# Kernel tuning notes

Hardware: AMD Instinct MI355X
Metric: run time of the kernel (lower is better)

Reference implementation:

```python
import jax, jax.numpy as jnp
import numpy as np

# Static problem sizes
N, NS, E, B = 6000, 20000, 60000, 16   # atoms, subgraph nodes, subgraph edges, molecules
IN_DIM, EMB, HID = 78, 1024, 2048
H = 4                 # GAT heads
C = HID // H          # 512 per-head channels
L = 3                 # num GAT layers
LN_EPS = 1e-5
SM_EPS = 1e-16        # PyG softmax denominator eps


def setup_inputs() -> dict:
    key = jax.random.key(0)
    ks = jax.random.split(key, 20)
    g = lambda k, shape, s: jax.random.normal(k, shape, jnp.float32) * s
    inp = {}
    inp["x"] = jax.random.uniform(ks[0], (N, IN_DIM), jnp.float32)
    inp["subgraph_edge_attr"] = jnp.ones((E, 1), jnp.float32)
    inp["Wn"] = g(ks[1], (IN_DIM, EMB), 0.1)
    inp["bn"] = g(ks[2], (EMB,), 0.02)
    inp["We"] = g(ks[3], (1, EMB), 0.1)
    inp["be"] = g(ks[4], (EMB,), 0.02)
    inp["W0"] = g(ks[5], (EMB, HID), EMB ** -0.5)
    inp["Ws"] = g(ks[6], (L - 1, HID, HID), HID ** -0.5)
    inp["att_src"] = g(ks[7], (L, H, C), C ** -0.5)
    inp["att_dst"] = g(ks[8], (L, H, C), C ** -0.5)
    inp["att_edge"] = g(ks[9], (L, H, C), C ** -0.5)
    inp["W_edge"] = g(ks[10], (L, EMB, HID), EMB ** -0.5)
    inp["conv_bias"] = g(ks[11], (L, HID), 0.02)
    inp["gamma"] = jnp.ones((L, HID), jnp.float32)
    inp["beta"] = jnp.zeros((L, HID), jnp.float32)
    inp["Wf"] = g(ks[12], (HID, HID), HID ** -0.5)
    inp["bf"] = g(ks[13], (HID,), 0.02)
    inp["subgraph_node_index"] = jax.random.randint(ks[14], (NS,), 0, N)
    inp["subgraph_edge_index"] = jax.random.randint(ks[15], (2, E), 0, NS)
    inp["subgraph_indicator"] = jax.random.randint(ks[16], (NS,), 0, N)
    inp["batch_index"] = jnp.sort(jax.random.randint(ks[17], (N,), 0, B))
    return inp


def _layernorm(h, g, b):
    mu = h.mean(-1, keepdims=True)
    v = jnp.square(h - mu).mean(-1, keepdims=True)
    return (h - mu) * jax.lax.rsqrt(v + LN_EPS) * g + b


def _gat_conv(h, Win, e_emb, a_src, a_dst, a_edge, We_l, bias, src, dst, n_nodes):
    # h: [n, in]; e_emb: [Et, EMB]; a_*: [H, C]
    xh = (h @ Win).reshape(-1, H, C)                       # [n, H, C]
    s_src = (xh * a_src).sum(-1)                           # [n, H]
    s_dst = (xh * a_dst).sum(-1)                           # [n, H]
    eh = (e_emb @ We_l).reshape(-1, H, C)                  # [Et, H, C]
    s_edge = (eh * a_edge).sum(-1)                         # [Et, H]
    logits = jax.nn.leaky_relu(s_src[src] + s_dst[dst] + s_edge, 0.2)
    # softmax over incoming edges of each destination node, per head
    m = jax.ops.segment_max(logits, dst, num_segments=n_nodes)
    p = jnp.exp(logits - m[dst])
    z = jax.ops.segment_sum(p, dst, num_segments=n_nodes)
    alpha = p / (z[dst] + SM_EPS)                          # [Et, H]
    msg = xh[src] * alpha[:, :, None]                      # [Et, H, C]
    out = jax.ops.segment_sum(msg, dst, num_segments=n_nodes)
    return out.reshape(-1, H * C) + bias                   # [n, HID]


def reference(x, subgraph_edge_attr, Wn, bn, We, be, W0, Ws, att_src, att_dst,
              att_edge, W_edge, conv_bias, gamma, beta, Wf, bf,
              subgraph_node_index, subgraph_edge_index, subgraph_indicator,
              batch_index):
    n_sub = subgraph_node_index.shape[0]
    n_nodes = x.shape[0]
    # node_projection + gather into subgraph-node space
    h = (x @ Wn + bn)[subgraph_node_index]                 # [NS, EMB]
    # edge_encoder
    e = subgraph_edge_attr @ We + be                       # [E, EMB]
    src = subgraph_edge_index[0]
    dst = subgraph_edge_index[1]
    # PyG GATConv add_self_loops with fill_value='mean' on encoded edge attrs
    loop = jnp.arange(n_sub)
    src = jnp.concatenate([src, loop])
    dst = jnp.concatenate([dst, loop])
    e_loop = jnp.broadcast_to(e.mean(axis=0, keepdims=True), (n_sub, e.shape[1]))
    e = jnp.concatenate([e, e_loop], axis=0)               # [E+NS, EMB]
    for i in range(L):
        Win = W0 if i == 0 else Ws[i - 1]
        h = _gat_conv(h, Win, e, att_src[i], att_dst[i], att_edge[i],
                      W_edge[i], conv_bias[i], src, dst, n_sub)
        h = jax.nn.relu(_layernorm(h, gamma[i], beta[i]))
    # subgraph mean aggregation back to atoms (index_add + bincount clamp(1))
    agg = jax.ops.segment_sum(h, subgraph_indicator, num_segments=n_nodes)
    cnt = jax.ops.segment_sum(jnp.ones((n_sub,), h.dtype), subgraph_indicator,
                              num_segments=n_nodes)
    agg = agg / jnp.maximum(cnt, 1.0)[:, None]
    out_nodes = agg @ Wf + bf                              # final_projection
    # global_mean_pool over molecules
    pooled = jax.ops.segment_sum(out_nodes, batch_index, num_segments=B)
    gcnt = jax.ops.segment_sum(jnp.ones((n_nodes,), h.dtype), batch_index,
                               num_segments=B)
    return pooled / jnp.maximum(gcnt, 1.0)[:, None]        # [B, HID]
```

## Files before the change

kernel.cpp:

```cpp
#include <hip/hip_runtime.h>

typedef unsigned short ushortT;
typedef __attribute__((ext_vector_type(4))) float f32x4;
typedef __attribute__((ext_vector_type(8))) short bf16x8;
typedef __attribute__((ext_vector_type(4))) unsigned int u32x4;
typedef __attribute__((ext_vector_type(4))) unsigned short u16x4;

#define N_ATOMS 6000
#define NSUB    20000
#define NEDGE   60000
#define NBATCH  16
#define INDIM   78
#define EMB     1024
#define HID     2048
#define NH      4
#define CH      512
#define NL      3
#define MP      20096
#define AP      6016
#define ETOT    (NEDGE + NSUB)
#define NPB     8

#define GLOAD_LDS16(gp, lp) \
    __builtin_amdgcn_global_load_lds((const __attribute__((address_space(1))) void*)(gp), \
                                     (__attribute__((address_space(3))) void*)(lp), 16, 0, 0)

__device__ __forceinline__ ushortT f2bf(float x) {
    union { float f; unsigned u; } v; v.f = x;
    unsigned r = v.u + 0x7fffu + ((v.u >> 16) & 1u);
    return (ushortT)(r >> 16);
}
__device__ __forceinline__ float bf2f(ushortT h) {
    union { unsigned u; float f; } v; v.u = ((unsigned)h) << 16; return v.f;
}

__global__ void k_cast_transpose(const float* __restrict__ W, ushortT* __restrict__ Wt,
                                 int K, int Nn) {
    __shared__ float tile[32][33];
    int n0 = blockIdx.x * 32, k0 = blockIdx.y * 32;
    int tx = threadIdx.x, ty = threadIdx.y;
    for (int i = 0; i < 32; i += 8)
        tile[ty + i][tx] = W[(size_t)(k0 + ty + i) * Nn + n0 + tx];
    __syncthreads();
    for (int i = 0; i < 32; i += 8)
        Wt[(size_t)(n0 + ty + i) * K + k0 + tx] = f2bf(tile[tx][ty + i]);
}

__global__ __launch_bounds__(256) void k_node_proj(const float* __restrict__ x,
                                                   const float* __restrict__ Wn,
                                                   const float* __restrict__ bn,
                                                   ushortT* __restrict__ xpb) {
    int n0 = blockIdx.x * NPB;
    __shared__ float xr[NPB][INDIM];
    int tid = threadIdx.x;
    for (int i = tid; i < NPB * INDIM; i += 256)
        xr[i / INDIM][i % INDIM] = x[(size_t)(n0 + i / INDIM) * INDIM + (i % INDIM)];
    __syncthreads();
    for (int j = tid; j < EMB; j += 256) {
        float acc[NPB];
        float b = bn[j];
        #pragma unroll
        for (int a = 0; a < NPB; ++a) acc[a] = b;
        #pragma unroll 6
        for (int k = 0; k < INDIM; ++k) {
            float wv = Wn[(size_t)k * EMB + j];
            #pragma unroll
            for (int a = 0; a < NPB; ++a) acc[a] += xr[a][k] * wv;
        }
        #pragma unroll
        for (int a = 0; a < NPB; ++a)
            xpb[(size_t)(n0 + a) * EMB + j] = f2bf(acc[a]);
    }
}

__global__ void k_mean_part(const float* __restrict__ ea, float* __restrict__ mpart) {
    __shared__ float red[256];
    int b = blockIdx.x;
    float s = 0;
    for (int i = b * 256 + threadIdx.x; i < NEDGE; i += 64 * 256) s += ea[i];
    red[threadIdx.x] = s; __syncthreads();
    for (int d = 128; d > 0; d >>= 1) {
        if (threadIdx.x < d) red[threadIdx.x] += red[threadIdx.x + d];
        __syncthreads();
    }
    if (threadIdx.x == 0) mpart[b] = red[0];
}

__global__ void k_eprep(const int* __restrict__ srci, const int* __restrict__ sni,
                        const float* __restrict__ ea, const float* __restrict__ meana,
                        int* __restrict__ esrcS, int* __restrict__ esrcA,
                        float* __restrict__ eaf) {
    int t = blockIdx.x * 256 + threadIdx.x;
    if (t >= ETOT) return;
    int s = (t < NEDGE) ? srci[t] : (t - NEDGE);
    esrcS[t] = s;
    esrcA[t] = sni[s];
    eaf[t] = (t < NEDGE) ? ea[t] : meana[0];
}

__global__ __launch_bounds__(256) void k_pq_part(const float* __restrict__ We,
                                                 const float* __restrict__ be,
                                                 const float* __restrict__ W_edge,
                                                 const float* __restrict__ att_edge,
                                                 float* __restrict__ part) {
    int l = blockIdx.x >> 2, h = blockIdx.x & 3;
    int k0 = blockIdx.y * 64;
    const float* Wl = W_edge + (size_t)l * EMB * HID + h * CH;
    const float* ae = att_edge + ((size_t)l * NH + h) * CH;
    int tid = threadIdx.x;
    float aP0 = 0, aP1 = 0, aQ0 = 0, aQ1 = 0;
    #pragma unroll 4
    for (int k = k0; k < k0 + 64; ++k) {
        float wek = We[k], bek = be[k];
        float w0 = Wl[(size_t)k * HID + tid];
        float w1 = Wl[(size_t)k * HID + tid + 256];
        aP0 += wek * w0; aP1 += wek * w1;
        aQ0 += bek * w0; aQ1 += bek * w1;
    }
    float p = aP0 * ae[tid] + aP1 * ae[tid + 256];
    float q = aQ0 * ae[tid] + aQ1 * ae[tid + 256];
    __shared__ float rp[256], rq[256];
    rp[tid] = p; rq[tid] = q; __syncthreads();
    for (int d = 128; d > 0; d >>= 1) {
        if (tid < d) { rp[tid] += rp[tid + d]; rq[tid] += rq[tid + d]; }
        __syncthreads();
    }
    if (tid == 0) {
        part[((size_t)blockIdx.y * 12 + blockIdx.x) * 2]     = rp[0];
        part[((size_t)blockIdx.y * 12 + blockIdx.x) * 2 + 1] = rq[0];
    }
}

__global__ void k_pq_red(const float* __restrict__ part, const float* __restrict__ mpart,
                         float* __restrict__ pq, float* __restrict__ meana) {
    int t = threadIdx.x;
    if (t < 24) {
        float s = 0;
        for (int kc = 0; kc < 16; ++kc) s += part[((size_t)kc * 12 + (t >> 1)) * 2 + (t & 1)];
        pq[t] = s;
    }
    if (t == 32) {
        float s = 0;
        for (int i = 0; i < 64; ++i) s += mpart[i];
        meana[0] = s / (float)NEDGE;
    }
}

__global__ void k_count(const int* __restrict__ dsti, int* __restrict__ cnt) {
    int t = blockIdx.x * 256 + threadIdx.x;
    if (t >= ETOT) return;
    int d = (t < NEDGE) ? dsti[t] : (t - NEDGE);
    atomicAdd(&cnt[d], 1);
}

__global__ void k_scan(const int* __restrict__ cnt, int* __restrict__ rs, int n) {
    __shared__ int part[1024];
    int tid = threadIdx.x;
    const int per = (n + 1023) / 1024;
    int base = tid * per;
    int s = 0;
    for (int i = 0; i < per; ++i) { int idx = base + i; if (idx < n) s += cnt[idx]; }
    part[tid] = s;
    __syncthreads();
    for (int d = 1; d < 1024; d <<= 1) {
        int v = (tid >= d) ? part[tid - d] : 0;
        __syncthreads();
        part[tid] += v;
        __syncthreads();
    }
    int off = part[tid] - s;
    for (int i = 0; i < per; ++i) {
        int idx = base + i;
        if (idx < n) { rs[idx] = off; off += cnt[idx]; }
    }
    if (tid == 1023) rs[n] = part[1023];
}

__global__ void k_fill(const int* __restrict__ dsti, const int* __restrict__ rs,
                       int* __restrict__ cursor, int* __restrict__ eids) {
    int t = blockIdx.x * 256 + threadIdx.x;
    if (t >= ETOT) return;
    int d = (t < NEDGE) ? dsti[t] : (t - NEDGE);
    int pos = rs[d] + atomicAdd(&cursor[d], 1);
    eids[pos] = t;
}

__global__ void k_count_ind(const int* __restrict__ ind, int* __restrict__ cnt) {
    int i = blockIdx.x * 256 + threadIdx.x;
    if (i < NSUB) atomicAdd(&cnt[ind[i]], 1);
}

__global__ void k_fill_ind(const int* __restrict__ ind, const int* __restrict__ rs,
                           int* __restrict__ cursor, int* __restrict__ ids) {
    int i = blockIdx.x * 256 + threadIdx.x;
    if (i >= NSUB) return;
    int a = ind[i];
    int pos = rs[a] + atomicAdd(&cursor[a], 1);
    ids[pos] = i;
}

__global__ __launch_bounds__(256) void k_gemm(const ushortT* __restrict__ A,
                                              const ushortT* __restrict__ Bt,
                                              ushortT* __restrict__ Cb, int K) {
    __shared__ alignas(16) ushortT As[128 * 64];
    __shared__ alignas(16) ushortT Bs[128 * 64];
    const int tid = threadIdx.x;
    const int nx = (int)gridDim.x;
    const int ny = (int)gridDim.y;
    int o = (int)blockIdx.y * nx + (int)blockIdx.x;
    int cpx = (nx * ny) >> 3;
    int s = (o & 7) * cpx + (o >> 3);
    const int bm = s / ny, bn = s % ny;
    const int wave = tid >> 6, lane = tid & 63;
    const int wr = wave >> 1, wc = wave & 1;
    f32x4 acc[4][4] = {};
    const int frow = lane & 15;
    const int cb0  = lane >> 4;
    const ushortT* Ab = A + (size_t)bm * 128 * K;
    const ushortT* Bb = Bt + (size_t)bn * 128 * K;
    const int srow = (lane >> 3);
    const int sswz = (((lane & 7) ^ srow) << 3);
    for (int k0 = 0; k0 < K; k0 += 64) {
        #pragma unroll
        for (int i = 0; i < 4; ++i) {
            int c = wave * 4 + i;
            int r = c * 8 + srow;
            GLOAD_LDS16(Ab + (size_t)r * K + k0 + sswz, As + c * 512 + lane * 8);
            GLOAD_LDS16(Bb + (size_t)r * K + k0 + sswz, Bs + c * 512 + lane * 8);
        }
        __syncthreads();
        #pragma unroll
        for (int kk = 0; kk < 64; kk += 32) {
            bf16x8 af[4], bfr[4];
            #pragma unroll
            for (int m = 0; m < 4; ++m) {
                int row = wr * 64 + m * 16 + frow;
                int cb = (kk >> 3) + cb0;
                af[m] = *(const bf16x8*)&As[row * 64 + ((cb ^ (frow & 7)) << 3)];
            }
            #pragma unroll
            for (int n = 0; n < 4; ++n) {
                int row = wc * 64 + n * 16 + frow;
                int cb = (kk >> 3) + cb0;
                bfr[n] = *(const bf16x8*)&Bs[row * 64 + ((cb ^ (frow & 7)) << 3)];
            }
            #pragma unroll
            for (int m = 0; m < 4; ++m)
                #pragma unroll
                for (int n = 0; n < 4; ++n)
                    acc[m][n] = __builtin_amdgcn_mfma_f32_16x16x32_bf16(af[m], bfr[n], acc[m][n], 0, 0, 0);
        }
        __syncthreads();
    }
    const int cr = (lane >> 4) * 4;
    const int cc = lane & 15;
    #pragma unroll
    for (int m = 0; m < 4; ++m)
        #pragma unroll
        for (int n = 0; n < 4; ++n)
            #pragma unroll
            for (int r = 0; r < 4; ++r) {
                size_t row = (size_t)bm * 128 + wr * 64 + m * 16 + cr + r;
                int col = bn * 128 + wc * 64 + n * 16 + cc;
                Cb[row * HID + col] = f2bf(acc[m][n][r]);
            }
}

__global__ __launch_bounds__(256) void k_sdots(const ushortT* __restrict__ xh,
                                               const float* __restrict__ att_src,
                                               const float* __restrict__ att_dst,
                                               float* __restrict__ ssrc,
                                               float* __restrict__ sdst, int layer) {
    int n = blockIdx.x;
    int h = threadIdx.x >> 6, lane = threadIdx.x & 63;
    const ushortT* row = xh + (size_t)n * HID + h * CH + lane * 8;
    const float* as = att_src + ((size_t)layer * NH + h) * CH + lane * 8;
    const float* ad = att_dst + ((size_t)layer * NH + h) * CH + lane * 8;
    u16x4 v0 = *(const u16x4*)row, v1 = *(const u16x4*)(row + 4);
    f32x4 a0 = *(const f32x4*)as, a1 = *(const f32x4*)(as + 4);
    f32x4 d0 = *(const f32x4*)ad, d1 = *(const f32x4*)(ad + 4);
    float ps = 0.f, pd = 0.f;
    #pragma unroll
    for (int t = 0; t < 4; ++t) {
        float f0 = bf2f(v0[t]), f1 = bf2f(v1[t]);
        ps += f0 * a0[t] + f1 * a1[t];
        pd += f0 * d0[t] + f1 * d1[t];
    }
    #pragma unroll
    for (int d = 32; d > 0; d >>= 1) { ps += __shfl_down(ps, d); pd += __shfl_down(pd, d); }
    if (lane == 0) { ssrc[n * NH + h] = ps; sdst[n * NH + h] = pd; }
}

__global__ __launch_bounds__(256) void k_attn(const ushortT* __restrict__ xh,
                                              const float* __restrict__ ssrc,
                                              const float* __restrict__ sdst,
                                              const int* __restrict__ rs,
                                              const int* __restrict__ eids,
                                              const int* __restrict__ esrc,
                                              const float* __restrict__ eaf,
                                              const float* __restrict__ pq,
                                              const float* __restrict__ conv_bias,
                                              const float* __restrict__ gammav,
                                              const float* __restrict__ betav,
                                              ushortT* __restrict__ hout, int layer,
                                              const int* __restrict__ nmap) {
    int wv = threadIdx.x >> 6, lane = threadIdx.x & 63;
    int n = blockIdx.x * 4 + wv;
    int nn = nmap ? nmap[n] : n;
    int beg = rs[n], end = rs[n + 1];
    float px[NH], qx[NH], sd[NH], m[NH], z[NH];
    #pragma unroll
    for (int h = 0; h < NH; ++h) {
        px[h] = pq[(layer * NH + h) * 2];
        qx[h] = pq[(layer * NH + h) * 2 + 1];
        sd[h] = sdst[nn * NH + h];
        m[h] = -INFINITY; z[h] = 0.f;
    }
    float facc[NH][8] = {};
    for (int pos = beg; pos < end; ++pos) {
        int t = eids[pos];
        int s = esrc[t];
        float a = eaf[t];
        const ushortT* xr = xh + (size_t)s * HID + lane * 8;
        #pragma unroll
        for (int h = 0; h < NH; ++h) {
            float logit = ssrc[s * NH + h] + sd[h] + a * px[h] + qx[h];
            logit = (logit > 0.f) ? logit : 0.2f * logit;
            float mn = fmaxf(m[h], logit);
            float scale = expf(m[h] - mn);
            float w = expf(logit - mn);
            z[h] = z[h] * scale + w;
            bf16x8 u = *(const bf16x8*)(xr + h * CH);
            #pragma unroll
            for (int j = 0; j < 8; ++j)
                facc[h][j] = facc[h][j] * scale + w * bf2f((ushortT)u[j]);
            m[h] = mn;
        }
    }
    float val[NH][8];
    float s1 = 0.f, s2 = 0.f;
    #pragma unroll
    for (int h = 0; h < NH; ++h) {
        float inv = 1.f / (z[h] + 1e-16f);
        int cb = h * CH + lane * 8;
        f32x4 b0 = *(const f32x4*)&conv_bias[layer * HID + cb];
        f32x4 b1 = *(const f32x4*)&conv_bias[layer * HID + cb + 4];
        #pragma unroll
        for (int j = 0; j < 4; ++j) {
            float v0 = facc[h][j] * inv + b0[j];
            float v1 = facc[h][4 + j] * inv + b1[j];
            val[h][j] = v0; val[h][4 + j] = v1;
            s1 += v0 + v1; s2 += v0 * v0 + v1 * v1;
        }
    }
    #pragma unroll
    for (int d = 32; d > 0; d >>= 1) { s1 += __shfl_xor(s1, d); s2 += __shfl_xor(s2, d); }
    float mu = s1 / (float)HID;
    float var = s2 / (float)HID - mu * mu;
    float rstd = rsqrtf(var + 1e-5f);
    #pragma unroll
    for (int h = 0; h < NH; ++h) {
        int cb = h * CH + lane * 8;
        f32x4 g0 = *(const f32x4*)&gammav[layer * HID + cb];
        f32x4 g1 = *(const f32x4*)&gammav[layer * HID + cb + 4];
        f32x4 e0 = *(const f32x4*)&betav[layer * HID + cb];
        f32x4 e1 = *(const f32x4*)&betav[layer * HID + cb + 4];
        u16x4 o0, o1;
        #pragma unroll
        for (int j = 0; j < 4; ++j) {
            float y0 = (val[h][j] - mu) * rstd * g0[j] + e0[j];
            float y1 = (val[h][4 + j] - mu) * rstd * g1[j] + e1[j];
            o0[j] = f2bf(fmaxf(y0, 0.f));
            o1[j] = f2bf(fmaxf(y1, 0.f));
        }
        *(u16x4*)&hout[(size_t)n * HID + cb]     = o0;
        *(u16x4*)&hout[(size_t)n * HID + cb + 4] = o1;
    }
}

__global__ __launch_bounds__(256) void k_agg(const ushortT* __restrict__ hbf,
                                             const int* __restrict__ rs2,
                                             const int* __restrict__ ids2,
                                             float* __restrict__ agg) {
    int a = blockIdx.x;
    int beg = rs2[a], end = rs2[a + 1];
    int col = threadIdx.x * 8;
    float acc[8] = {0,0,0,0,0,0,0,0};
    for (int pos = beg; pos < end; ++pos) {
        int i = ids2[pos];
        const u16x4* ptr = (const u16x4*)(hbf + (size_t)i * HID + col);
        u16x4 h0 = ptr[0], h1 = ptr[1];
        #pragma unroll
        for (int t = 0; t < 4; ++t) { acc[t] += bf2f(h0[t]); acc[4 + t] += bf2f(h1[t]); }
    }
    int cnt = end - beg;
    float inv = 1.f / (float)(cnt > 1 ? cnt : 1);
    f32x4 o0, o1;
    #pragma unroll
    for (int t = 0; t < 4; ++t) { o0[t] = acc[t] * inv; o1[t] = acc[4 + t] * inv; }
    float* dst = agg + (size_t)a * HID + col;
    *(f32x4*)dst = o0;
    *(f32x4*)(dst + 4) = o1;
}

__global__ void k_branges(const int* __restrict__ batch, int* __restrict__ bstart,
                          int* __restrict__ bend) {
    int a = blockIdx.x * 256 + threadIdx.x;
    if (a < N_ATOMS) {
        int b = batch[a];
        atomicMin(&bstart[b], a);
        atomicMax(&bend[b], a + 1);
    }
}

__global__ __launch_bounds__(128) void k_pool(const float* __restrict__ agg,
                                              const int* __restrict__ bstart,
                                              const int* __restrict__ bend,
                                              float* __restrict__ pa) {
    int b = blockIdx.x;
    int col = blockIdx.y * 128 + threadIdx.x;
    int s = bstart[b], e = bend[b];
    float v = 0.f;
    for (int a = s; a < e; ++a) v += agg[(size_t)a * HID + col];
    int g = e - s;
    pa[b * HID + col] = (g > 0) ? v / (float)g : 0.f;
}

__global__ __launch_bounds__(256) void k_fpart(const float* __restrict__ pa,
                                               const float* __restrict__ Wf,
                                               float* __restrict__ part) {
    int kc = blockIdx.x;
    int col = blockIdx.y * 256 + threadIdx.x;
    int k0 = kc * 128;
    __shared__ float pl[NBATCH][128];
    for (int i = threadIdx.x; i < NBATCH * 128; i += 256) {
        int b = i >> 7, k = i & 127;
        pl[b][k] = pa[b * HID + k0 + k];
    }
    __syncthreads();
    float acc[NBATCH];
    #pragma unroll
    for (int b = 0; b < NBATCH; ++b) acc[b] = 0.f;
    for (int kk = 0; kk < 128; kk += 4) {
        f32x4 w;
        #pragma unroll
        for (int u = 0; u < 4; ++u) w[u] = Wf[(size_t)(k0 + kk + u) * HID + col];
        #pragma unroll
        for (int b = 0; b < NBATCH; ++b) {
            f32x4 pv = *(const f32x4*)&pl[b][kk];
            acc[b] += pv[0] * w[0] + pv[1] * w[1] + pv[2] * w[2] + pv[3] * w[3];
        }
    }
    #pragma unroll
    for (int b = 0; b < NBATCH; ++b)
        part[((size_t)kc * NBATCH + b) * HID + col] = acc[b];
}

__global__ __launch_bounds__(256) void k_fred(const float* __restrict__ part,
                                              const float* __restrict__ bfv,
                                              const int* __restrict__ bstart,
                                              const int* __restrict__ bend,
                                              float* __restrict__ out) {
    int b = blockIdx.x;
    int col = blockIdx.y * 256 + threadIdx.x;
    float s = 0.f;
    #pragma unroll
    for (int kc = 0; kc < 16; ++kc)
        s += part[((size_t)kc * NBATCH + b) * HID + col];
    int g = bend[b] - bstart[b];
    out[b * HID + col] = (g > 0) ? s + bfv[col] : 0.f;
}

extern "C" void kernel_launch(void* const* d_in, const int* in_sizes, int n_in,
                              void* d_out, int out_size, void* d_ws, size_t ws_size,
                              hipStream_t stream) {
    const float* x         = (const float*)d_in[0];
    const float* ea        = (const float*)d_in[1];
    const float* Wn        = (const float*)d_in[2];
    const float* bn        = (const float*)d_in[3];
    const float* We        = (const float*)d_in[4];
    const float* be        = (const float*)d_in[5];
    const float* W0        = (const float*)d_in[6];
    const float* Ws        = (const float*)d_in[7];
    const float* att_src   = (const float*)d_in[8];
    const float* att_dst   = (const float*)d_in[9];
    const float* att_edge  = (const float*)d_in[10];
    const float* W_edge    = (const float*)d_in[11];
    const float* conv_bias = (const float*)d_in[12];
    const float* gammav    = (const float*)d_in[13];
    const float* betav     = (const float*)d_in[14];
    const float* Wf        = (const float*)d_in[15];
    const float* bfv       = (const float*)d_in[16];
    const int* sni         = (const int*)d_in[17];
    const int* sei         = (const int*)d_in[18];
    const int* sind        = (const int*)d_in[19];
    const int* batch       = (const int*)d_in[20];
    float* out = (float*)d_out;

    char* p = (char*)d_ws;
    auto carve = [&](size_t bytes) -> char* {
        char* r = p; p += (bytes + 255) & ~(size_t)255; return r;
    };
    ushortT* Wt0   = (ushortT*)carve((size_t)HID * EMB * 2);
    ushortT* Wt1   = (ushortT*)carve((size_t)HID * HID * 2);
    ushortT* Wt2   = (ushortT*)carve((size_t)HID * HID * 2);
    ushortT* xpb   = (ushortT*)carve((size_t)AP * EMB * 2);
    ushortT* xha   = (ushortT*)carve((size_t)AP * HID * 2);
    ushortT* hbf   = (ushortT*)carve((size_t)MP * HID * 2);
    ushortT* xhb   = (ushortT*)carve((size_t)MP * HID * 2);
    float*   ssrc  = (float*)carve((size_t)MP * NH * 4);
    float*   sdstb = (float*)carve((size_t)MP * NH * 4);
    float*   ssrca = (float*)carve((size_t)AP * NH * 4);
    float*   sdsta = (float*)carve((size_t)AP * NH * 4);
    float*   pq    = (float*)carve(NL * NH * 2 * 4);
    float*   meana = (float*)carve(256);
    float*   pqpart= (float*)carve((size_t)16 * 12 * 2 * 4);
    float*   mpart = (float*)carve(64 * 4);
    int*     cntdeg= (int*)carve((size_t)NSUB * 4);
    int*     rs    = (int*)carve((size_t)(NSUB + 1) * 4);
    int*     cursor= (int*)carve((size_t)NSUB * 4);
    int*     eids  = (int*)carve((size_t)ETOT * 4);
    int*     esrcS = (int*)carve((size_t)ETOT * 4);
    int*     esrcA = (int*)carve((size_t)ETOT * 4);
    float*   eaf   = (float*)carve((size_t)ETOT * 4);
    int*     cnt2  = (int*)carve((size_t)N_ATOMS * 4);
    int*     rs2   = (int*)carve((size_t)(N_ATOMS + 1) * 4);
    int*     cur2  = (int*)carve((size_t)N_ATOMS * 4);
    int*     ids2  = (int*)carve((size_t)NSUB * 4);
    int*     bstart= (int*)carve(NBATCH * 4);
    int*     bend  = (int*)carve(NBATCH * 4);
    float*   pa    = (float*)carve((size_t)NBATCH * HID * 4);
    float*   part  = (float*)carve((size_t)16 * NBATCH * HID * 4);
    float*   agg   = (float*)xhb;

    hipMemsetAsync(hbf + (size_t)NSUB * HID, 0, (size_t)(MP - NSUB) * HID * 2, stream);
    hipMemsetAsync(xpb + (size_t)N_ATOMS * EMB, 0, (size_t)(AP - N_ATOMS) * EMB * 2, stream);
    hipMemsetAsync(cntdeg, 0, (size_t)NSUB * 4, stream);
    hipMemsetAsync(cursor, 0, (size_t)NSUB * 4, stream);
    hipMemsetAsync(cnt2, 0, (size_t)N_ATOMS * 4, stream);
    hipMemsetAsync(cur2, 0, (size_t)N_ATOMS * 4, stream);
    hipMemsetAsync(bstart, 0x7f, NBATCH * 4, stream);
    hipMemsetAsync(bend, 0, NBATCH * 4, stream);

    dim3 tb(32, 8);
    k_cast_transpose<<<dim3(HID / 32, EMB / 32), tb, 0, stream>>>(W0, Wt0, EMB, HID);
    k_cast_transpose<<<dim3(HID / 32, HID / 32), tb, 0, stream>>>(Ws, Wt1, HID, HID);
    k_cast_transpose<<<dim3(HID / 32, HID / 32), tb, 0, stream>>>(Ws + (size_t)HID * HID, Wt2, HID, HID);

    k_node_proj<<<N_ATOMS / NPB, 256, 0, stream>>>(x, Wn, bn, xpb);
    k_mean_part<<<64, 256, 0, stream>>>(ea, mpart);
    k_pq_part<<<dim3(NL * NH, 16), 256, 0, stream>>>(We, be, W_edge, att_edge, pqpart);
    k_pq_red<<<1, 64, 0, stream>>>(pqpart, mpart, pq, meana);

    const int* dsti = sei + NEDGE;
    k_eprep<<<(ETOT + 255) / 256, 256, 0, stream>>>(sei, sni, ea, meana, esrcS, esrcA, eaf);
    k_count<<<(ETOT + 255) / 256, 256, 0, stream>>>(dsti, cntdeg);
    k_scan<<<1, 1024, 0, stream>>>(cntdeg, rs, NSUB);
    k_fill<<<(ETOT + 255) / 256, 256, 0, stream>>>(dsti, rs, cursor, eids);
    k_count_ind<<<(NSUB + 255) / 256, 256, 0, stream>>>(sind, cnt2);
    k_scan<<<1, 1024, 0, stream>>>(cnt2, rs2, N_ATOMS);
    k_fill_ind<<<(NSUB + 255) / 256, 256, 0, stream>>>(sind, rs2, cur2, ids2);
    k_branges<<<(N_ATOMS + 255) / 256, 256, 0, stream>>>(batch, bstart, bend);

    k_gemm<<<dim3(AP / 128, HID / 128), 256, 0, stream>>>(xpb, Wt0, xha, EMB);
    k_sdots<<<N_ATOMS, 256, 0, stream>>>(xha, att_src, att_dst, ssrca, sdsta, 0);
    k_attn<<<NSUB / 4, 256, 0, stream>>>(xha, ssrca, sdsta, rs, eids, esrcA, eaf, pq,
                                         conv_bias, gammav, betav, hbf, 0, sni);

    for (int l = 1; l < NL; ++l) {
        const ushortT* Wt = (l == 1) ? Wt1 : Wt2;
        k_gemm<<<dim3(MP / 128, HID / 128), 256, 0, stream>>>(hbf, Wt, xhb, HID);
        k_sdots<<<NSUB, 256, 0, stream>>>(xhb, att_src, att_dst, ssrc, sdstb, l);
        k_attn<<<NSUB / 4, 256, 0, stream>>>(xhb, ssrc, sdstb, rs, eids, esrcS, eaf, pq,
                                             conv_bias, gammav, betav, hbf, l, (const int*)nullptr);
    }

    k_agg<<<N_ATOMS, 256, 0, stream>>>(hbf, rs2, ids2, agg);
    k_pool<<<dim3(NBATCH, HID / 128), 128, 0, stream>>>(agg, bstart, bend, pa);
    k_fpart<<<dim3(16, HID / 256), 256, 0, stream>>>(pa, Wf, part);
    k_fred<<<dim3(NBATCH, HID / 256), 256, 0, stream>>>(part, bfv, bstart, bend, out);
}
```

Measured before the change: 997.2 us.

## Fuse preprocessing kernels and store edge data in CSR order for attention

Merges the three weight cast-transposes into one 3D-grid launch. Folds the count, fill, edge-prep and batch-range kernels into two combined kernels. The fill step now writes source index and edge attribute straight into destination-sorted (CSR) order, so the attention loop no longer goes through an extra eids indirection. The attention kernel also loads pq, sdst and ssrc as float4 vectors, and the padding-row memsets for hbf and xpb are removed. The removed memsets leave the GEMM padding rows uninitialized, which relies on those rows never being consumed.

```diff
diff --git a/kernel.cpp b/kernel.cpp
--- a/kernel.cpp
+++ b/kernel.cpp
@@ -34,13 +34,19 @@
     union { unsigned u; float f; } v; v.u = ((unsigned)h) << 16; return v.f;
 }
 
-__global__ void k_cast_transpose(const float* __restrict__ W, ushortT* __restrict__ Wt,
-                                 int K, int Nn) {
+__global__ void k_cast3(const float* __restrict__ W0, const float* __restrict__ Ws,
+                        ushortT* __restrict__ Wt0, ushortT* __restrict__ Wt1,
+                        ushortT* __restrict__ Wt2) {
     __shared__ float tile[32][33];
+    int z = blockIdx.z;
+    const float* W = (z == 0) ? W0 : (z == 1 ? Ws : Ws + (size_t)HID * HID);
+    ushortT* Wt = (z == 0) ? Wt0 : (z == 1 ? Wt1 : Wt2);
+    int K = (z == 0) ? EMB : HID;
     int n0 = blockIdx.x * 32, k0 = blockIdx.y * 32;
+    if (k0 >= K) return;
     int tx = threadIdx.x, ty = threadIdx.y;
     for (int i = 0; i < 32; i += 8)
-        tile[ty + i][tx] = W[(size_t)(k0 + ty + i) * Nn + n0 + tx];
+        tile[ty + i][tx] = W[(size_t)(k0 + ty + i) * HID + n0 + tx];
     __syncthreads();
     for (int i = 0; i < 32; i += 8)
         Wt[(size_t)(n0 + ty + i) * K + k0 + tx] = f2bf(tile[tx][ty + i]);
@@ -84,18 +90,6 @@
         __syncthreads();
     }
     if (threadIdx.x == 0) mpart[b] = red[0];
-}
-
-__global__ void k_eprep(const int* __restrict__ srci, const int* __restrict__ sni,
-                        const float* __restrict__ ea, const float* __restrict__ meana,
-                        int* __restrict__ esrcS, int* __restrict__ esrcA,
-                        float* __restrict__ eaf) {
-    int t = blockIdx.x * 256 + threadIdx.x;
-    if (t >= ETOT) return;
-    int s = (t < NEDGE) ? srci[t] : (t - NEDGE);
-    esrcS[t] = s;
-    esrcA[t] = sni[s];
-    eaf[t] = (t < NEDGE) ? ea[t] : meana[0];
 }
 
 __global__ __launch_bounds__(256) void k_pq_part(const float* __restrict__ We,
@@ -146,11 +140,22 @@
     }
 }
 
-__global__ void k_count(const int* __restrict__ dsti, int* __restrict__ cnt) {
+__global__ void k_counts(const int* __restrict__ dsti, const int* __restrict__ sind,
+                         const int* __restrict__ batch,
+                         int* __restrict__ cntdeg, int* __restrict__ cnt2,
+                         int* __restrict__ bstart, int* __restrict__ bend) {
     int t = blockIdx.x * 256 + threadIdx.x;
-    if (t >= ETOT) return;
-    int d = (t < NEDGE) ? dsti[t] : (t - NEDGE);
-    atomicAdd(&cnt[d], 1);
+    if (t < ETOT) {
+        int d = (t < NEDGE) ? dsti[t] : (t - NEDGE);
+        atomicAdd(&cntdeg[d], 1);
+    } else if (t < ETOT + NSUB) {
+        atomicAdd(&cnt2[sind[t - ETOT]], 1);
+    } else if (t < ETOT + NSUB + N_ATOMS) {
+        int a = t - ETOT - NSUB;
+        int b = batch[a];
+        atomicMin(&bstart[b], a);
+        atomicMax(&bend[b], a + 1);
+    }
 }
 
 __global__ void k_scan(const int* __restrict__ cnt, int* __restrict__ rs, int n) {
@@ -176,27 +181,28 @@
     if (tid == 1023) rs[n] = part[1023];
 }
 
-__global__ void k_fill(const int* __restrict__ dsti, const int* __restrict__ rs,
-                       int* __restrict__ cursor, int* __restrict__ eids) {
+__global__ void k_fills(const int* __restrict__ dsti, const int* __restrict__ srci,
+                        const int* __restrict__ sni, const float* __restrict__ ea,
+                        const float* __restrict__ meana, const int* __restrict__ sind,
+                        const int* __restrict__ rs, const int* __restrict__ rs2,
+                        int* __restrict__ cursor, int* __restrict__ cur2,
+                        int* __restrict__ esrcPS, int* __restrict__ esrcPA,
+                        float* __restrict__ eafP, int* __restrict__ ids2) {
     int t = blockIdx.x * 256 + threadIdx.x;
-    if (t >= ETOT) return;
-    int d = (t < NEDGE) ? dsti[t] : (t - NEDGE);
-    int pos = rs[d] + atomicAdd(&cursor[d], 1);
-    eids[pos] = t;
-}
-
-__global__ void k_count_ind(const int* __restrict__ ind, int* __restrict__ cnt) {
-    int i = blockIdx.x * 256 + threadIdx.x;
-    if (i < NSUB) atomicAdd(&cnt[ind[i]], 1);
-}
-
-__global__ void k_fill_ind(const int* __restrict__ ind, const int* __restrict__ rs,
-                           int* __restrict__ cursor, int* __restrict__ ids) {
-    int i = blockIdx.x * 256 + threadIdx.x;
-    if (i >= NSUB) return;
-    int a = ind[i];
-    int pos = rs[a] + atomicAdd(&cursor[a], 1);
-    ids[pos] = i;
+    if (t < ETOT) {
+        int d, s; float a;
+        if (t < NEDGE) { d = dsti[t]; s = srci[t]; a = ea[t]; }
+        else           { d = t - NEDGE; s = d;     a = meana[0]; }
+        int pos = rs[d] + atomicAdd(&cursor[d], 1);
+        esrcPS[pos] = s;
+        esrcPA[pos] = sni[s];
+        eafP[pos] = a;
+    } else if (t < ETOT + NSUB) {
+        int i = t - ETOT;
+        int aT = sind[i];
+        int pos = rs2[aT] + atomicAdd(&cur2[aT], 1);
+        ids2[pos] = i;
+    }
 }
 
 __global__ __launch_bounds__(256) void k_gemm(const ushortT* __restrict__ A,
@@ -295,9 +301,8 @@
                                               const float* __restrict__ ssrc,
                                               const float* __restrict__ sdst,
                                               const int* __restrict__ rs,
-                                              const int* __restrict__ eids,
-                                              const int* __restrict__ esrc,
-                                              const float* __restrict__ eaf,
+                                              const int* __restrict__ esrcP,
+                                              const float* __restrict__ eafP,
                                               const float* __restrict__ pq,
                                               const float* __restrict__ conv_bias,
                                               const float* __restrict__ gammav,
@@ -308,23 +313,23 @@
     int n = blockIdx.x * 4 + wv;
     int nn = nmap ? nmap[n] : n;
     int beg = rs[n], end = rs[n + 1];
-    float px[NH], qx[NH], sd[NH], m[NH], z[NH];
-    #pragma unroll
-    for (int h = 0; h < NH; ++h) {
-        px[h] = pq[(layer * NH + h) * 2];
-        qx[h] = pq[(layer * NH + h) * 2 + 1];
-        sd[h] = sdst[nn * NH + h];
-        m[h] = -INFINITY; z[h] = 0.f;
-    }
+    f32x4 pq01 = *(const f32x4*)&pq[layer * 8];
+    f32x4 pq23 = *(const f32x4*)&pq[layer * 8 + 4];
+    float px[NH] = {pq01[0], pq01[2], pq23[0], pq23[2]};
+    float qx[NH] = {pq01[1], pq01[3], pq23[1], pq23[3]};
+    f32x4 sdv = *(const f32x4*)&sdst[nn * NH];
+    float m[NH], z[NH];
+    #pragma unroll
+    for (int h = 0; h < NH; ++h) { m[h] = -INFINITY; z[h] = 0.f; }
     float facc[NH][8] = {};
     for (int pos = beg; pos < end; ++pos) {
-        int t = eids[pos];
-        int s = esrc[t];
-        float a = eaf[t];
+        int s = esrcP[pos];
+        float a = eafP[pos];
+        f32x4 ssv = *(const f32x4*)&ssrc[s * NH];
         const ushortT* xr = xh + (size_t)s * HID + lane * 8;
         #pragma unroll
         for (int h = 0; h < NH; ++h) {
-            float logit = ssrc[s * NH + h] + sd[h] + a * px[h] + qx[h];
+            float logit = ssv[h] + sdv[h] + a * px[h] + qx[h];
             logit = (logit > 0.f) ? logit : 0.2f * logit;
             float mn = fmaxf(m[h], logit);
             float scale = expf(m[h] - mn);
@@ -401,16 +406,6 @@
     float* dst = agg + (size_t)a * HID + col;
     *(f32x4*)dst = o0;
     *(f32x4*)(dst + 4) = o1;
-}
-
-__global__ void k_branges(const int* __restrict__ batch, int* __restrict__ bstart,
-                          int* __restrict__ bend) {
-    int a = blockIdx.x * 256 + threadIdx.x;
-    if (a < N_ATOMS) {
-        int b = batch[a];
-        atomicMin(&bstart[b], a);
-        atomicMax(&bend[b], a + 1);
-    }
 }
 
 __global__ __launch_bounds__(128) void k_pool(const float* __restrict__ agg,
@@ -519,10 +514,9 @@
     int*     cntdeg= (int*)carve((size_t)NSUB * 4);
     int*     rs    = (int*)carve((size_t)(NSUB + 1) * 4);
     int*     cursor= (int*)carve((size_t)NSUB * 4);
-    int*     eids  = (int*)carve((size_t)ETOT * 4);
-    int*     esrcS = (int*)carve((size_t)ETOT * 4);
-    int*     esrcA = (int*)carve((size_t)ETOT * 4);
-    float*   eaf   = (float*)carve((size_t)ETOT * 4);
+    int*     esrcPS= (int*)carve((size_t)ETOT * 4);
+    int*     esrcPA= (int*)carve((size_t)ETOT * 4);
+    float*   eafP  = (float*)carve((size_t)ETOT * 4);
     int*     cnt2  = (int*)carve((size_t)N_ATOMS * 4);
     int*     rs2   = (int*)carve((size_t)(N_ATOMS + 1) * 4);
     int*     cur2  = (int*)carve((size_t)N_ATOMS * 4);
@@ -533,45 +527,39 @@
     float*   part  = (float*)carve((size_t)16 * NBATCH * HID * 4);
     float*   agg   = (float*)xhb;
 
-    hipMemsetAsync(hbf + (size_t)NSUB * HID, 0, (size_t)(MP - NSUB) * HID * 2, stream);
-    hipMemsetAsync(xpb + (size_t)N_ATOMS * EMB, 0, (size_t)(AP - N_ATOMS) * EMB * 2, stream);
-    hipMemsetAsync(cntdeg, 0, (size_t)NSUB * 4, stream);
-    hipMemsetAsync(cursor, 0, (size_t)NSUB * 4, stream);
-    hipMemsetAsync(cnt2, 0, (size_t)N_ATOMS * 4, stream);
-    hipMemsetAsync(cur2, 0, (size_t)N_ATOMS * 4, stream);
-    hipMemsetAsync(bstart, 0x7f, NBATCH * 4, stream);
-    hipMemsetAsync(bend, 0, NBATCH * 4, stream);
+    (void)hipMemsetAsync(cntdeg, 0, (size_t)NSUB * 4, stream);
+    (void)hipMemsetAsync(cursor, 0, (size_t)NSUB * 4, stream);
+    (void)hipMemsetAsync(cnt2, 0, (size_t)N_ATOMS * 4, stream);
+    (void)hipMemsetAsync(cur2, 0, (size_t)N_ATOMS * 4, stream);
+    (void)hipMemsetAsync(bstart, 0x7f, NBATCH * 4, stream);
+    (void)hipMemsetAsync(bend, 0, NBATCH * 4, stream);
 
     dim3 tb(32, 8);
-    k_cast_transpose<<<dim3(HID / 32, EMB / 32), tb, 0, stream>>>(W0, Wt0, EMB, HID);
-    k_cast_transpose<<<dim3(HID / 32, HID / 32), tb, 0, stream>>>(Ws, Wt1, HID, HID);
-    k_cast_transpose<<<dim3(HID / 32, HID / 32), tb, 0, stream>>>(Ws + (size_t)HID * HID, Wt2, HID, HID);
-
+    k_cast3<<<dim3(HID / 32, HID / 32, 3), tb, 0, stream>>>(W0, Ws, Wt0, Wt1, Wt2);
     k_node_proj<<<N_ATOMS / NPB, 256, 0, stream>>>(x, Wn, bn, xpb);
     k_mean_part<<<64, 256, 0, stream>>>(ea, mpart);
     k_pq_part<<<dim3(NL * NH, 16), 256, 0, stream>>>(We, be, W_edge, att_edge, pqpart);
     k_pq_red<<<1, 64, 0, stream>>>(pqpart, mpart, pq, meana);
 
     const int* dsti = sei + NEDGE;
-    k_eprep<<<(ETOT + 255) / 256, 256, 0, stream>>>(sei, sni, ea, meana, esrcS, esrcA, eaf);
-    k_count<<<(ETOT + 255) / 256, 256, 0, stream>>>(dsti, cntdeg);
+    k_counts<<<(ETOT + NSUB + N_ATOMS + 255) / 256, 256, 0, stream>>>(
+        dsti, sind, batch, cntdeg, cnt2, bstart, bend);
     k_scan<<<1, 1024, 0, stream>>>(cntdeg, rs, NSUB);
-    k_fill<<<(ETOT + 255) / 256, 256, 0, stream>>>(dsti, rs, cursor, eids);
-    k_count_ind<<<(NSUB + 255) / 256, 256, 0, stream>>>(sind, cnt2);
     k_scan<<<1, 1024, 0, stream>>>(cnt2, rs2, N_ATOMS);
-    k_fill_ind<<<(NSUB + 255) / 256, 256, 0, stream>>>(sind, rs2, cur2, ids2);
-    k_branges<<<(N_ATOMS + 255) / 256, 256, 0, stream>>>(batch, bstart, bend);
+    k_fills<<<(ETOT + NSUB + 255) / 256, 256, 0, stream>>>(
+        dsti, sei, sni, ea, meana, sind, rs, rs2, cursor, cur2,
+        esrcPS, esrcPA, eafP, ids2);
 
     k_gemm<<<dim3(AP / 128, HID / 128), 256, 0, stream>>>(xpb, Wt0, xha, EMB);
     k_sdots<<<N_ATOMS, 256, 0, stream>>>(xha, att_src, att_dst, ssrca, sdsta, 0);
-    k_attn<<<NSUB / 4, 256, 0, stream>>>(xha, ssrca, sdsta, rs, eids, esrcA, eaf, pq,
+    k_attn<<<NSUB / 4, 256, 0, stream>>>(xha, ssrca, sdsta, rs, esrcPA, eafP, pq,
                                          conv_bias, gammav, betav, hbf, 0, sni);
 
     for (int l = 1; l < NL; ++l) {
         const ushortT* Wt = (l == 1) ? Wt1 : Wt2;
         k_gemm<<<dim3(MP / 128, HID / 128), 256, 0, stream>>>(hbf, Wt, xhb, HID);
         k_sdots<<<NSUB, 256, 0, stream>>>(xhb, att_src, att_dst, ssrc, sdstb, l);
-        k_attn<<<NSUB / 4, 256, 0, stream>>>(xhb, ssrc, sdstb, rs, eids, esrcS, eaf, pq,
+        k_attn<<<NSUB / 4, 256, 0, stream>>>(xhb, ssrc, sdstb, rs, esrcPS, eafP, pq,
                                              conv_bias, gammav, betav, hbf, l, (const int*)nullptr);
     }
 
```

Measured after the change: 957.1 us. -4.0%, faster.
